# Kernel optimization log

Measured on AMD Instinct MI355X. Metric: run time of the kernel, lower is better.

Reference implementation:

```python
import jax, jax.numpy as jnp
import numpy as np

N_NODES = 100000
N_EDGES = 1600000
IN_C, HID_C, OUT_C = 64, 64, 32


def setup_inputs() -> dict:
    key = jax.random.key(0)
    ks = jax.random.split(key, 6)
    x = jax.random.normal(ks[0], (N_NODES, IN_C), dtype=jnp.float32)
    edge_index = jax.random.randint(ks[1], (2, N_EDGES), 0, N_NODES, dtype=jnp.int64)
    edge_weight = jax.random.uniform(ks[2], (N_EDGES,), dtype=jnp.float32)
    # Glorot-ish init for the two GCNConv weight matrices, zero bias (PyG default)
    W1 = jax.random.normal(ks[3], (IN_C, HID_C), dtype=jnp.float32) / np.sqrt(IN_C)
    b1 = jnp.zeros((HID_C,), dtype=jnp.float32)
    W2 = jax.random.normal(ks[4], (HID_C, OUT_C), dtype=jnp.float32) / np.sqrt(HID_C)
    b2 = jnp.zeros((OUT_C,), dtype=jnp.float32)
    return {"x": x, "edge_index": edge_index, "edge_weight": edge_weight,
            "W1": W1, "b1": b1, "W2": W2, "b2": b2}


def _gcn_conv(x, src, dst, w, W, b):
    """PyG GCNConv: add self-loops (weight 1), symmetric D^-1/2 (A+I) D^-1/2 norm,
    then aggregate transformed features into destination nodes, plus bias."""
    n = x.shape[0]
    loop = jnp.arange(n, dtype=src.dtype)
    s = jnp.concatenate([src, loop])
    d = jnp.concatenate([dst, loop])
    wl = jnp.concatenate([w, jnp.ones((n,), dtype=x.dtype)])
    deg = jax.ops.segment_sum(wl, d, num_segments=n)            # [N]
    dinv = jnp.where(deg > 0, jax.lax.rsqrt(deg), 0.0)
    norm = dinv[s] * wl * dinv[d]                               # [E+N]
    xw = x @ W                                                  # [N, C_out]
    msg = norm[:, None] * xw[s]                                 # gather + scale
    return jax.ops.segment_sum(msg, d, num_segments=n) + b      # scatter-add


def reference(x, edge_index, edge_weight, W1, b1, W2, b2):
    src, dst = edge_index[0], edge_index[1]
    h = _gcn_conv(x, src, dst, edge_weight, W1, b1)
    h = jax.nn.relu(h)
    # dropout(p=0.5, training=self.training): identity in eval mode
    return _gcn_conv(h, src, dst, edge_weight, W2, b2)
```

## Files before the change

kernel.cpp:

```cpp
#include <hip/hip_runtime.h>

#define N_NODES 100000
#define N_EDGES 1600000
#define IN_C 64
#define HID_C 64
#define OUT_C 32

#define NB 391
#define BSHIFT 8
#define BMASK 255
#define SEG_CAP 4864
#define EPB 4096
#define BIN_BLOCKS ((N_EDGES + EPB - 1) / EPB)
#define SMASK 0x1FFFF
#define FIXSCALE 34359738368.0f

__device__ __forceinline__ unsigned int bpack(float a, float b) {
    unsigned int ua = __float_as_uint(a);
    ua += 0x7FFFu + ((ua >> 16) & 1u);
    unsigned int ub = __float_as_uint(b);
    ub += 0x7FFFu + ((ub >> 16) & 1u);
    return (ua >> 16) | (ub & 0xFFFF0000u);
}
__device__ __forceinline__ float2 bup(unsigned int v) {
    return make_float2(__uint_as_float(v << 16), __uint_as_float(v & 0xFFFF0000u));
}


__global__ void __launch_bounds__(256) bin_kernel(const int* __restrict__ src,
                                                  const int* __restrict__ dst,
                                                  const float* __restrict__ w,
                                                  int* __restrict__ gcnt,
                                                  int2* __restrict__ seg) {
    __shared__ int2 recs[EPB];
    __shared__ int meta[EPB];
    __shared__ int hist[NB];
    __shared__ int gbase[NB];
    int tid = threadIdx.x;
    for (int i = tid; i < NB; i += 256) hist[i] = 0;
    __syncthreads();
    int e0 = blockIdx.x * EPB;
    int n = min(EPB, N_EDGES - e0);
    for (int i = tid; i < n; i += 256) {
        int d = dst[e0 + i];
        int b = d >> BSHIFT;
        recs[i] = make_int2(src[e0 + i] | ((d & BMASK) << 17), __float_as_int(w[e0 + i]));
        int rank = atomicAdd(&hist[b], 1);
        meta[i] = b | (rank << 9);
    }
    __syncthreads();
    for (int b = tid; b < NB; b += 256) {
        int c = hist[b];
        gbase[b] = c ? atomicAdd(&gcnt[b], c) : 0;
    }
    __syncthreads();
    for (int i = tid; i < n; i += 256) {
        int m = meta[i];
        int b = m & 511, rank = m >> 9;
        int pos = gbase[b] + rank;
        if (pos < SEG_CAP) seg[(size_t)b * SEG_CAP + pos] = recs[i];
    }
}


__global__ void __launch_bounds__(256) bsort_kernel(const int* __restrict__ gcnt,
                                                    const int2* __restrict__ seg,
                                                    int2* __restrict__ seg2,
                                                    float* __restrict__ dinv,
                                                    int2* __restrict__ rowRC) {
    __shared__ int2 recs[SEG_CAP];
    __shared__ unsigned long long packed[256];
    __shared__ int meta[SEG_CAP];
    __shared__ int sarr[256];
    __shared__ int ofs0[256];
    int tid = threadIdx.x, b = blockIdx.x;
    int n = min(gcnt[b], SEG_CAP);
    const int2* sp = seg + (size_t)b * SEG_CAP;
    packed[tid] = 0ULL;
    __syncthreads();
    for (int i = tid; i < n; i += 256) {
        int2 r = sp[i];
        recs[i] = r;
        int dl = (r.x >> 17) & BMASK;
        unsigned long long fixw =
            (unsigned long long)(__int_as_float(r.y) * FIXSCALE);
        unsigned long long old = atomicAdd(&packed[dl], (1ULL << 48) | fixw);
        meta[i] = dl | ((int)(old >> 48) << 8);
    }
    __syncthreads();
    unsigned long long p = packed[tid];
    int myc = (int)(p >> 48);
    float degw = (float)((double)(p & ((1ULL << 48) - 1)) * (1.0 / (double)FIXSCALE));
    int node = (b << BSHIFT) + tid;
    if (node < N_NODES) dinv[node] = rsqrtf(1.0f + degw);
    int padc = (myc + 1) & ~1;
    sarr[tid] = padc;
    __syncthreads();
    for (int off = 1; off < 256; off <<= 1) {
        int tmp = (tid >= off) ? sarr[tid - off] : 0;
        __syncthreads();
        sarr[tid] += tmp;
        __syncthreads();
    }
    int excl = sarr[tid] - padc;
    if (node < N_NODES) rowRC[node] = make_int2(b * SEG_CAP + excl, myc);
    ofs0[tid] = excl;
    __syncthreads();
    int2* op = seg2 + (size_t)b * SEG_CAP;
    for (int i = tid; i < n; i += 256) {
        int m = meta[i];
        int dl = m & BMASK, rank = m >> 8;
        op[ofs0[dl] + rank] = recs[i];
    }
}


__global__ void __launch_bounds__(256) gemm1_kernel(const float* __restrict__ X,
                                                    const float* __restrict__ W,
                                                    const float* __restrict__ dinv,
                                                    unsigned int* __restrict__ XWs,
                                                    int nRows) {
    __shared__ float XsT[64][64];
    __shared__ float Ws[64][64];
    int tid = threadIdx.x;
    {
        const float4* Wv = (const float4*)W;
        float4* Wsv = (float4*)&Ws[0][0];
        for (int i = tid; i < 1024; i += 256) Wsv[i] = Wv[i];
    }
    int row0 = blockIdx.x * 64;
    int rmax = nRows - row0;
    for (int i = tid; i < 64 * 16; i += 256) {
        int r = i >> 4, kq = i & 15;
        float4 v = (r < rmax) ? ((const float4*)(X + (size_t)(row0 + r) * IN_C))[kq]
                              : make_float4(0.f, 0.f, 0.f, 0.f);
        XsT[4 * kq + 0][r] = v.x;
        XsT[4 * kq + 1][r] = v.y;
        XsT[4 * kq + 2][r] = v.z;
        XsT[4 * kq + 3][r] = v.w;
    }
    __syncthreads();
    int tr = tid >> 4, tc = tid & 15;
    float acc[4][4] = {};
    float a[4], bb[4];
#pragma unroll 8
    for (int k = 0; k < 64; ++k) {
        *(float4*)a = *(const float4*)&XsT[k][4 * tr];
        *(float4*)bb = *(const float4*)&Ws[k][4 * tc];
#pragma unroll
        for (int i = 0; i < 4; ++i)
#pragma unroll
            for (int j = 0; j < 4; ++j) acc[i][j] += a[i] * bb[j];
    }
#pragma unroll
    for (int i = 0; i < 4; ++i) {
        int rl = 4 * tr + i;
        if (rl < rmax) {
            int row = row0 + rl;
            float di = dinv[row];
            uint2 o;
            o.x = bpack(acc[i][0] * di, acc[i][1] * di);
            o.y = bpack(acc[i][2] * di, acc[i][3] * di);
            ((uint2*)XWs)[(size_t)row * 16 + tc] = o;
        }
    }
}


__global__ void __launch_bounds__(256) agg1_kernel(const int2* __restrict__ rowRC,
                                                   const int2* __restrict__ seg2,
                                                   const unsigned int* __restrict__ XWs,
                                                   const float* __restrict__ dinv,
                                                   const float* __restrict__ b1,
                                                   float* __restrict__ H) {
    int l32 = threadIdx.x & 31;
    int d = blockIdx.x * 8 + (threadIdx.x >> 5);
    if (d >= N_NODES) return;
    float did = dinv[d];
    float2 bv = ((const float2*)b1)[l32];
    float2 s2 = bup(XWs[(size_t)d * 32 + l32]);
    float ax = bv.x + did * s2.x, ay = bv.y + did * s2.y;
    int2 rc = rowRC[d];
    int nc = rc.y;
    const int2* sp = seg2 + rc.x;
    const int4* sp4 = (const int4*)sp;
    int e = 0;
    for (; e + 8 <= nc; e += 8) {
        int4 q0 = sp4[(e >> 1) + 0], q1 = sp4[(e >> 1) + 1];
        int4 q2 = sp4[(e >> 1) + 2], q3 = sp4[(e >> 1) + 3];
        int s0 = q0.x & SMASK, s1 = q0.z & SMASK, s4 = q1.x & SMASK, s5 = q1.z & SMASK;
        int s6 = q2.x & SMASK, s7 = q2.z & SMASK, s8 = q3.x & SMASK, s9 = q3.z & SMASK;
        unsigned int r0 = XWs[(size_t)s0 * 32 + l32];
        unsigned int r1 = XWs[(size_t)s1 * 32 + l32];
        unsigned int r2 = XWs[(size_t)s4 * 32 + l32];
        unsigned int r3 = XWs[(size_t)s5 * 32 + l32];
        unsigned int r4 = XWs[(size_t)s6 * 32 + l32];
        unsigned int r5 = XWs[(size_t)s7 * 32 + l32];
        unsigned int r6 = XWs[(size_t)s8 * 32 + l32];
        unsigned int r7 = XWs[(size_t)s9 * 32 + l32];
        float c0 = __int_as_float(q0.y) * did, c1 = __int_as_float(q0.w) * did;
        float c2 = __int_as_float(q1.y) * did, c3 = __int_as_float(q1.w) * did;
        float c4 = __int_as_float(q2.y) * did, c5 = __int_as_float(q2.w) * did;
        float c6 = __int_as_float(q3.y) * did, c7 = __int_as_float(q3.w) * did;
        float2 v;
        v = bup(r0); ax += c0 * v.x; ay += c0 * v.y;
        v = bup(r1); ax += c1 * v.x; ay += c1 * v.y;
        v = bup(r2); ax += c2 * v.x; ay += c2 * v.y;
        v = bup(r3); ax += c3 * v.x; ay += c3 * v.y;
        v = bup(r4); ax += c4 * v.x; ay += c4 * v.y;
        v = bup(r5); ax += c5 * v.x; ay += c5 * v.y;
        v = bup(r6); ax += c6 * v.x; ay += c6 * v.y;
        v = bup(r7); ax += c7 * v.x; ay += c7 * v.y;
    }
    for (; e + 2 <= nc; e += 2) {
        int4 q = sp4[e >> 1];
        int s0 = q.x & SMASK, s1 = q.z & SMASK;
        unsigned int r0 = XWs[(size_t)s0 * 32 + l32];
        unsigned int r1 = XWs[(size_t)s1 * 32 + l32];
        float c0 = __int_as_float(q.y) * did, c1 = __int_as_float(q.w) * did;
        float2 v;
        v = bup(r0); ax += c0 * v.x; ay += c0 * v.y;
        v = bup(r1); ax += c1 * v.x; ay += c1 * v.y;
    }
    if (e < nc) {
        int2 p = sp[e];
        int s = p.x & SMASK;
        float c = __int_as_float(p.y) * did;
        float2 v = bup(XWs[(size_t)s * 32 + l32]);
        ax += c * v.x;
        ay += c * v.y;
    }
    ((float2*)H)[(size_t)d * 32 + l32] = make_float2(fmaxf(ax, 0.f), fmaxf(ay, 0.f));
}


__global__ void __launch_bounds__(256) gemm2_kernel(const float* __restrict__ H,
                                                    const float* __restrict__ W,
                                                    const float* __restrict__ dinv,
                                                    unsigned int* __restrict__ HWs,
                                                    int nRows) {
    __shared__ float HsT[64][128];
    __shared__ float Ws[64][32];
    int tid = threadIdx.x;
    {
        const float4* Wv = (const float4*)W;
        float4* Wsv = (float4*)&Ws[0][0];
        for (int i = tid; i < 512; i += 256) Wsv[i] = Wv[i];
    }
    int row0 = blockIdx.x * 128;
    int rmax = nRows - row0;
    for (int i = tid; i < 128 * 16; i += 256) {
        int r = i >> 4, kq = i & 15;
        float4 v = (r < rmax) ? ((const float4*)(H + (size_t)(row0 + r) * HID_C))[kq]
                              : make_float4(0.f, 0.f, 0.f, 0.f);
        HsT[4 * kq + 0][r] = v.x;
        HsT[4 * kq + 1][r] = v.y;
        HsT[4 * kq + 2][r] = v.z;
        HsT[4 * kq + 3][r] = v.w;
    }
    __syncthreads();
    int tr = tid >> 3, tc = tid & 7;
    float acc[4][4] = {};
    float a[4], bb[4];
#pragma unroll 8
    for (int k = 0; k < 64; ++k) {
        *(float4*)a = *(const float4*)&HsT[k][4 * tr];
        *(float4*)bb = *(const float4*)&Ws[k][4 * tc];
#pragma unroll
        for (int i = 0; i < 4; ++i)
#pragma unroll
            for (int j = 0; j < 4; ++j) acc[i][j] += a[i] * bb[j];
    }
#pragma unroll
    for (int i = 0; i < 4; ++i) {
        int rl = 4 * tr + i;
        if (rl < rmax) {
            int row = row0 + rl;
            float di = dinv[row];
            uint2 o;
            o.x = bpack(acc[i][0] * di, acc[i][1] * di);
            o.y = bpack(acc[i][2] * di, acc[i][3] * di);
            ((uint2*)HWs)[(size_t)row * 8 + tc] = o;
        }
    }
}


__global__ void __launch_bounds__(256) agg2_kernel(const int2* __restrict__ rowRC,
                                                   const int2* __restrict__ seg2,
                                                   const unsigned int* __restrict__ HWs,
                                                   const float* __restrict__ dinv,
                                                   const float* __restrict__ b2,
                                                   float* __restrict__ out) {
    int l16 = threadIdx.x & 15;
    int d = blockIdx.x * 16 + (threadIdx.x >> 4);
    if (d >= N_NODES) return;
    float did = dinv[d];
    float2 bv = ((const float2*)b2)[l16];
    float2 s2 = bup(HWs[(size_t)d * 16 + l16]);
    float ax = bv.x + did * s2.x, ay = bv.y + did * s2.y;
    int2 rc = rowRC[d];
    int nc = rc.y;
    const int2* sp = seg2 + rc.x;
    const int4* sp4 = (const int4*)sp;
    int e = 0;
    for (; e + 8 <= nc; e += 8) {
        int4 q0 = sp4[(e >> 1) + 0], q1 = sp4[(e >> 1) + 1];
        int4 q2 = sp4[(e >> 1) + 2], q3 = sp4[(e >> 1) + 3];
        int s0 = q0.x & SMASK, s1 = q0.z & SMASK, s4 = q1.x & SMASK, s5 = q1.z & SMASK;
        int s6 = q2.x & SMASK, s7 = q2.z & SMASK, s8 = q3.x & SMASK, s9 = q3.z & SMASK;
        unsigned int r0 = HWs[(size_t)s0 * 16 + l16];
        unsigned int r1 = HWs[(size_t)s1 * 16 + l16];
        unsigned int r2 = HWs[(size_t)s4 * 16 + l16];
        unsigned int r3 = HWs[(size_t)s5 * 16 + l16];
        unsigned int r4 = HWs[(size_t)s6 * 16 + l16];
        unsigned int r5 = HWs[(size_t)s7 * 16 + l16];
        unsigned int r6 = HWs[(size_t)s8 * 16 + l16];
        unsigned int r7 = HWs[(size_t)s9 * 16 + l16];
        float c0 = __int_as_float(q0.y) * did, c1 = __int_as_float(q0.w) * did;
        float c2 = __int_as_float(q1.y) * did, c3 = __int_as_float(q1.w) * did;
        float c4 = __int_as_float(q2.y) * did, c5 = __int_as_float(q2.w) * did;
        float c6 = __int_as_float(q3.y) * did, c7 = __int_as_float(q3.w) * did;
        float2 v;
        v = bup(r0); ax += c0 * v.x; ay += c0 * v.y;
        v = bup(r1); ax += c1 * v.x; ay += c1 * v.y;
        v = bup(r2); ax += c2 * v.x; ay += c2 * v.y;
        v = bup(r3); ax += c3 * v.x; ay += c3 * v.y;
        v = bup(r4); ax += c4 * v.x; ay += c4 * v.y;
        v = bup(r5); ax += c5 * v.x; ay += c5 * v.y;
        v = bup(r6); ax += c6 * v.x; ay += c6 * v.y;
        v = bup(r7); ax += c7 * v.x; ay += c7 * v.y;
    }
    for (; e + 2 <= nc; e += 2) {
        int4 q = sp4[e >> 1];
        int s0 = q.x & SMASK, s1 = q.z & SMASK;
        unsigned int r0 = HWs[(size_t)s0 * 16 + l16];
        unsigned int r1 = HWs[(size_t)s1 * 16 + l16];
        float c0 = __int_as_float(q.y) * did, c1 = __int_as_float(q.w) * did;
        float2 v;
        v = bup(r0); ax += c0 * v.x; ay += c0 * v.y;
        v = bup(r1); ax += c1 * v.x; ay += c1 * v.y;
    }
    if (e < nc) {
        int2 p = sp[e];
        int s = p.x & SMASK;
        float c = __int_as_float(p.y) * did;
        float2 v = bup(HWs[(size_t)s * 16 + l16]);
        ax += c * v.x;
        ay += c * v.y;
    }
    ((float2*)out)[(size_t)d * 16 + l16] = make_float2(ax, ay);
}


extern "C" void kernel_launch(void* const* d_in, const int* in_sizes, int n_in,
                              void* d_out, int out_size, void* d_ws, size_t ws_size,
                              hipStream_t stream) {
    const float* x = (const float*)d_in[0];
    const int* edge_index = (const int*)d_in[1];
    const float* ew = (const float*)d_in[2];
    const float* W1 = (const float*)d_in[3];
    const float* b1 = (const float*)d_in[4];
    const float* W2 = (const float*)d_in[5];
    const float* b2 = (const float*)d_in[6];
    float* out = (float*)d_out;

    const int* src = edge_index;
    const int* dst = edge_index + N_EDGES;

    char* ws = (char*)d_ws;
    size_t off = 0;
    auto carve = [&](size_t bytes) -> void* {
        void* p = ws + off;
        off += (bytes + 255) & ~(size_t)255;
        return p;
    };

    int* gcnt = (int*)carve(NB * 4);
    float* dinv = (float*)carve((size_t)N_NODES * 4);
    int2* rowRC = (int2*)carve((size_t)N_NODES * 8);
    int2* seg = (int2*)carve((size_t)NB * SEG_CAP * 8);
    int2* seg2 = (int2*)carve((size_t)NB * SEG_CAP * 8);
    unsigned int* XWs = (unsigned int*)carve((size_t)N_NODES * 32 * 4);
    float* H = (float*)carve((size_t)N_NODES * HID_C * 4);
    unsigned int* HWs = XWs;

    hipMemsetAsync(gcnt, 0, NB * 4, stream);
    bin_kernel<<<BIN_BLOCKS, 256, 0, stream>>>(src, dst, ew, gcnt, seg);
    bsort_kernel<<<NB, 256, 0, stream>>>(gcnt, seg, seg2, dinv, rowRC);
    gemm1_kernel<<<(N_NODES + 63) / 64, 256, 0, stream>>>(x, W1, dinv, XWs, N_NODES);
    agg1_kernel<<<(N_NODES + 7) / 8, 256, 0, stream>>>(rowRC, seg2, XWs, dinv, b1, H);
    gemm2_kernel<<<(N_NODES + 127) / 128, 256, 0, stream>>>(H, W2, dinv, HWs, N_NODES);
    agg2_kernel<<<(N_NODES + 15) / 16, 256, 0, stream>>>(rowRC, seg2, HWs, dinv, b2, out);
}
```

Measured before the change: 227.8 us.

## Store hidden activations as bf16, vectorize edge binning loads, remap gemm1 tile loads

The first-layer aggregation output H is now packed to bf16 pairs, which halves its write in agg1 and its read in gemm2; gemm2 unpacks the values into its shared-memory tile. bin_kernel now reads src, dst and weight as 4-wide vectors and processes four edges per iteration. gemm1's tile load is remapped so consecutive threads take consecutive rows, changing the order of shared-memory stores. Rounding H to bf16 adds precision loss before the second layer, and the vector loads assume the per-block edge count is a multiple of 4, which holds for these sizes.

```diff
diff --git a/kernel.cpp b/kernel.cpp
--- a/kernel.cpp
+++ b/kernel.cpp
@@ -41,12 +41,28 @@
     __syncthreads();
     int e0 = blockIdx.x * EPB;
     int n = min(EPB, N_EDGES - e0);
-    for (int i = tid; i < n; i += 256) {
-        int d = dst[e0 + i];
-        int b = d >> BSHIFT;
-        recs[i] = make_int2(src[e0 + i] | ((d & BMASK) << 17), __float_as_int(w[e0 + i]));
-        int rank = atomicAdd(&hist[b], 1);
-        meta[i] = b | (rank << 9);
+    const int4* src4 = (const int4*)(src + e0);
+    const int4* dst4 = (const int4*)(dst + e0);
+    const float4* w4 = (const float4*)(w + e0);
+    int n4 = n >> 2;
+    for (int i = tid; i < n4; i += 256) {
+        int4 s = src4[i];
+        int4 d = dst4[i];
+        float4 ww = w4[i];
+        int j = i << 2;
+#define BIN_ONE(K, SS, DD, WW)                                             \
+        {                                                                  \
+            int b = (DD) >> BSHIFT;                                        \
+            recs[j + K] = make_int2((SS) | (((DD) & BMASK) << 17),         \
+                                    __float_as_int(WW));                   \
+            int rank = atomicAdd(&hist[b], 1);                             \
+            meta[j + K] = b | (rank << 9);                                 \
+        }
+        BIN_ONE(0, s.x, d.x, ww.x)
+        BIN_ONE(1, s.y, d.y, ww.y)
+        BIN_ONE(2, s.z, d.z, ww.z)
+        BIN_ONE(3, s.w, d.w, ww.w)
+#undef BIN_ONE
     }
     __syncthreads();
     for (int b = tid; b < NB; b += 256) {
@@ -131,7 +147,7 @@
     int row0 = blockIdx.x * 64;
     int rmax = nRows - row0;
     for (int i = tid; i < 64 * 16; i += 256) {
-        int r = i >> 4, kq = i & 15;
+        int r = i & 63, kq = i >> 6;
         float4 v = (r < rmax) ? ((const float4*)(X + (size_t)(row0 + r) * IN_C))[kq]
                               : make_float4(0.f, 0.f, 0.f, 0.f);
         XsT[4 * kq + 0][r] = v.x;
@@ -172,7 +188,7 @@
                                                    const unsigned int* __restrict__ XWs,
                                                    const float* __restrict__ dinv,
                                                    const float* __restrict__ b1,
-                                                   float* __restrict__ H) {
+                                                   unsigned int* __restrict__ Hb) {
     int l32 = threadIdx.x & 31;
     int d = blockIdx.x * 8 + (threadIdx.x >> 5);
     if (d >= N_NODES) return;
@@ -230,11 +246,11 @@
         ax += c * v.x;
         ay += c * v.y;
     }
-    ((float2*)H)[(size_t)d * 32 + l32] = make_float2(fmaxf(ax, 0.f), fmaxf(ay, 0.f));
-}
-
-
-__global__ void __launch_bounds__(256) gemm2_kernel(const float* __restrict__ H,
+    Hb[(size_t)d * 32 + l32] = bpack(fmaxf(ax, 0.f), fmaxf(ay, 0.f));
+}
+
+
+__global__ void __launch_bounds__(256) gemm2_kernel(const unsigned int* __restrict__ Hb,
                                                     const float* __restrict__ W,
                                                     const float* __restrict__ dinv,
                                                     unsigned int* __restrict__ HWs,
@@ -249,14 +265,15 @@
     }
     int row0 = blockIdx.x * 128;
     int rmax = nRows - row0;
-    for (int i = tid; i < 128 * 16; i += 256) {
-        int r = i >> 4, kq = i & 15;
-        float4 v = (r < rmax) ? ((const float4*)(H + (size_t)(row0 + r) * HID_C))[kq]
-                              : make_float4(0.f, 0.f, 0.f, 0.f);
-        HsT[4 * kq + 0][r] = v.x;
-        HsT[4 * kq + 1][r] = v.y;
-        HsT[4 * kq + 2][r] = v.z;
-        HsT[4 * kq + 3][r] = v.w;
+    for (int i = tid; i < 128 * 8; i += 256) {
+        int r = i & 127, kq = i >> 7;
+        uint4 v = (r < rmax) ? ((const uint4*)(Hb + (size_t)(row0 + r) * 32))[kq]
+                             : make_uint4(0u, 0u, 0u, 0u);
+        float2 f;
+        f = bup(v.x); HsT[8 * kq + 0][r] = f.x; HsT[8 * kq + 1][r] = f.y;
+        f = bup(v.y); HsT[8 * kq + 2][r] = f.x; HsT[8 * kq + 3][r] = f.y;
+        f = bup(v.z); HsT[8 * kq + 4][r] = f.x; HsT[8 * kq + 5][r] = f.y;
+        f = bup(v.w); HsT[8 * kq + 6][r] = f.x; HsT[8 * kq + 7][r] = f.y;
     }
     __syncthreads();
     int tr = tid >> 3, tc = tid & 7;
@@ -382,14 +399,14 @@
     int2* seg = (int2*)carve((size_t)NB * SEG_CAP * 8);
     int2* seg2 = (int2*)carve((size_t)NB * SEG_CAP * 8);
     unsigned int* XWs = (unsigned int*)carve((size_t)N_NODES * 32 * 4);
-    float* H = (float*)carve((size_t)N_NODES * HID_C * 4);
+    unsigned int* Hb = (unsigned int*)carve((size_t)N_NODES * 32 * 4);
     unsigned int* HWs = XWs;
 
     hipMemsetAsync(gcnt, 0, NB * 4, stream);
     bin_kernel<<<BIN_BLOCKS, 256, 0, stream>>>(src, dst, ew, gcnt, seg);
     bsort_kernel<<<NB, 256, 0, stream>>>(gcnt, seg, seg2, dinv, rowRC);
     gemm1_kernel<<<(N_NODES + 63) / 64, 256, 0, stream>>>(x, W1, dinv, XWs, N_NODES);
-    agg1_kernel<<<(N_NODES + 7) / 8, 256, 0, stream>>>(rowRC, seg2, XWs, dinv, b1, H);
-    gemm2_kernel<<<(N_NODES + 127) / 128, 256, 0, stream>>>(H, W2, dinv, HWs, N_NODES);
+    agg1_kernel<<<(N_NODES + 7) / 8, 256, 0, stream>>>(rowRC, seg2, XWs, dinv, b1, Hb);
+    gemm2_kernel<<<(N_NODES + 127) / 128, 256, 0, stream>>>(Hb, W2, dinv, HWs, N_NODES);
     agg2_kernel<<<(N_NODES + 15) / 16, 256, 0, stream>>>(rowRC, seg2, HWs, dinv, b2, out);
 }
```

Result: no change. 224.4 us (-1.5%).
